# Kernel tuning notes

Hardware: AMD Instinct MI355X
Metric: run time of the kernel (lower is better)

## Reference

```python
import jax, jax.numpy as jnp
import numpy as np

B, T, I, H, P = 256, 2048, 2, 128, 129  # batch, max_len, input feats, hidden, num_pitches


def setup_inputs() -> dict:
    key = jax.random.key(0)
    ks = jax.random.split(key, 8)
    s = 1.0 / np.sqrt(H)  # torch LSTM/Linear init scale
    x = jax.random.normal(ks[0], (B, T, I), jnp.float32)
    lengths = jax.random.randint(ks[1], (B,), 1, T + 1, jnp.int32)
    W_ih = jax.random.uniform(ks[2], (4 * H, I), jnp.float32, -s, s)
    W_hh = jax.random.uniform(ks[3], (4 * H, H), jnp.float32, -s, s)
    note_W = jax.random.uniform(ks[4], (P, H), jnp.float32, -s, s)
    note_b = jax.random.uniform(ks[5], (P,), jnp.float32, -s, s)
    dur_W = jax.random.uniform(ks[6], (1, H), jnp.float32, -s, s)
    dur_b = jax.random.uniform(ks[7], (1,), jnp.float32, -s, s)
    return dict(x=x, lengths=lengths, W_ih=W_ih, W_hh=W_hh,
                note_W=note_W, note_b=note_b, dur_W=dur_W, dur_b=dur_b)


def _lstm(x, lengths, W_ih, W_hh):
    # Precompute input projections for all timesteps in one GEMM: [T,B,4H]
    pre = jnp.einsum('bti,gi->tbg', x, W_ih)
    h0 = jnp.zeros((x.shape[0], W_hh.shape[1]), x.dtype)
    c0 = h0
    ts = jnp.arange(x.shape[1])

    def step(carry, inp):
        h, c = carry
        px, t = inp
        gates = px + h @ W_hh.T  # [B,4H], torch gate order: i,f,g,o
        i_g, f_g, g_g, o_g = jnp.split(gates, 4, axis=-1)
        i_g = jax.nn.sigmoid(i_g)
        f_g = jax.nn.sigmoid(f_g)
        o_g = jax.nn.sigmoid(o_g)
        g_g = jnp.tanh(g_g)
        c_new = f_g * c + i_g * g_g
        h_new = o_g * jnp.tanh(c_new)
        m = (t < lengths)[:, None]  # packed semantics: freeze past length
        h2 = jnp.where(m, h_new, h)
        c2 = jnp.where(m, c_new, c)
        return (h2, c2), jnp.where(m, h_new, 0.0)

    (hT, cT), hs = jax.lax.scan(step, (h0, c0), (pre, ts))
    return jnp.transpose(hs, (1, 0, 2)), hT, cT  # [B,T,H], final states = states at last valid step


def reference(x, lengths, W_ih, W_hh, note_W, note_b, dur_W, dur_b):
    hs, hT, cT = _lstm(x, lengths, W_ih, W_hh)
    mask = (jnp.arange(x.shape[1])[None, :] < lengths[:, None])[..., None]
    note_logits = jnp.where(mask, hs @ note_W.T + note_b, 0.0)     # [B,T,129]
    duration_pred = jnp.where(mask, hs @ dur_W.T + dur_b, 0.0)     # [B,T,1]
    return note_logits, duration_pred, hT, cT
```

## Files before the change

### kernel.cpp

```cpp
#include <hip/hip_runtime.h>


typedef _Float16 f16;
typedef _Float16 f16x8 __attribute__((ext_vector_type(8)));
typedef float    f32x4 __attribute__((ext_vector_type(4)));

#define B_  256
#define T_  2048
#define H_  128
#define P_  129

static constexpr size_t NOTE_N   = (size_t)B_ * T_ * P_;
static constexpr size_t DUR_BASE = NOTE_N;
static constexpr size_t HT_BASE  = DUR_BASE + (size_t)B_ * T_;
static constexpr size_t CT_BASE  = HT_BASE + (size_t)B_ * H_;

#if defined(__has_builtin)
#if __has_builtin(__builtin_amdgcn_exp2f)
#define EXP2F(x) __builtin_amdgcn_exp2f(x)
#endif
#endif
#ifndef EXP2F
#define EXP2F(x) __expf((x) * 0.6931471805599453f)
#endif

__device__ __forceinline__ float fast_rcp(float x) { return __builtin_amdgcn_rcpf(x); }

__device__ __forceinline__ float sigmoid_f(float x) {
    float e = EXP2F(-1.44269504f * x);
    return fast_rcp(1.f + e);
}
__device__ __forceinline__ float tanh_f(float x) {
    float e = EXP2F(2.885390082f * x);
    return (e - 1.f) * fast_rcp(e + 1.f);
}

__device__ __forceinline__ f16* hs_row(float* out, int bt) {
    size_t byteoff = ((size_t)bt * (P_ * 4) + 15) & ~(size_t)15;
    return (f16*)((char*)out + byteoff);
}

__global__ __launch_bounds__(256) void prep_k(const float* __restrict__ note_W,
                                              const float* __restrict__ dur_W,
                                              f16* __restrict__ Wn) {
    int i = threadIdx.x + blockIdx.x * 256;
    if (i >= 144 * 128) return;
    int row = i >> 7, k = i & 127;
    float v = 0.f;
    if (row < 129)       v = note_W[row * 128 + k];
    else if (row == 129) v = dur_W[k];
    Wn[i] = (f16)v;
}

__global__ __launch_bounds__(256, 1) void lstm4_k(const float* __restrict__ x,
                                                  const int* __restrict__ lengths,
                                                  const float* __restrict__ W_ih,
                                                  const float* __restrict__ W_hh,
                                                  float* __restrict__ out) {
    __shared__ __align__(16) f16 h_sh[2][H_];
    __shared__ __align__(8) float2 xs[128];

    const int tid = threadIdx.x;
    const int b = blockIdx.x;
    const int w = tid >> 6;
    const int l = tid & 63;
    const int p = l & 15;
    const int q = l >> 4;
    const int sel = q >> 1;
    const int j = 16 * w + 64 * sel + p;
    const bool writer = ((q & 1) == 0);

    f16x8 Bf[8][4];
    float wxx[8], wxy[8];
#pragma unroll
    for (int s = 0; s < 8; s++) {
        const int c = 16 * (w + 4 * s) + p;
        const float* wr = W_hh + (size_t)c * H_ + 8 * q;
#pragma unroll
        for (int kt = 0; kt < 4; kt++) {
            float4 v1 = *(const float4*)(wr + 32 * kt);
            float4 v2 = *(const float4*)(wr + 32 * kt + 4);
            f16x8 f;
            f[0] = (f16)v1.x; f[1] = (f16)v1.y; f[2] = (f16)v1.z; f[3] = (f16)v1.w;
            f[4] = (f16)v2.x; f[5] = (f16)v2.y; f[6] = (f16)v2.z; f[7] = (f16)v2.w;
            Bf[s][kt] = f;
        }
        wxx[s] = W_ih[2 * c];
        wxy[s] = W_ih[2 * c + 1];
    }
    const int len = lengths[b];
    if (tid < 2 * H_) ((f16*)h_sh)[tid] = (f16)0.f;

    char* hp = (char*)out + (size_t)b * (T_ * 516ULL) + 2 * j;

    const f32x4 z4 = {0.f, 0.f, 0.f, 0.f};
    float c_reg = 0.f, h_reg = 0.f;

    for (int t = 0; t < len; t++) {
        if ((t & 127) == 0) {
            __syncthreads();
            if (tid < 128)
                xs[tid] = *(const float2*)(x + (size_t)b * T_ * 2 + (size_t)(t + tid) * 2);
            __syncthreads();
        }
        const int cur = t & 1;

        f16x8 Af[4];
#pragma unroll
        for (int kt = 0; kt < 4; kt++)
            Af[kt] = *(const f16x8*)(&h_sh[cur][32 * kt + 8 * q]);

        f32x4 acc[8];
#pragma unroll
        for (int s = 0; s < 8; s++)
            acc[s] = __builtin_amdgcn_mfma_f32_16x16x32_f16(Af[0], Bf[s][0], z4, 0, 0, 0);
#pragma unroll
        for (int kt = 1; kt < 4; kt++) {
#pragma unroll
            for (int s = 0; s < 8; s++)
                acc[s] = __builtin_amdgcn_mfma_f32_16x16x32_f16(
                    Af[kt], Bf[s][kt], acc[s], 0, 0, 0);
        }

        const float2 xv = xs[t & 127];
        float G[4];
#pragma unroll
        for (int tt = 0; tt < 4; tt++) {
            float ga = acc[2 * tt][0] +
                       __builtin_fmaf(wxy[2 * tt], xv.y, wxx[2 * tt] * xv.x);
            float gb = acc[2 * tt + 1][0] +
                       __builtin_fmaf(wxy[2 * tt + 1], xv.y, wxx[2 * tt + 1] * xv.x);
            G[tt] = sel ? gb : ga;
        }

        const float ig = sigmoid_f(G[0]);
        const float fg = sigmoid_f(G[1]);
        const float gg = tanh_f(G[2]);
        const float og = sigmoid_f(G[3]);
        c_reg = __builtin_fmaf(fg, c_reg, ig * gg);
        h_reg = og * tanh_f(fminf(fmaxf(c_reg, -15.f), 15.f));

        if (writer) {
            const f16 h16 = (f16)h_reg;
            h_sh[cur ^ 1][j] = h16;
            *(f16*)hp = h16;
        }
        hp += 512 + (((t & 3) == 0) ? 16 : 0);

        asm volatile("s_waitcnt lgkmcnt(0)" ::: "memory");
        __builtin_amdgcn_sched_barrier(0);
        __builtin_amdgcn_s_barrier();
        __builtin_amdgcn_sched_barrier(0);
    }

    if (writer) {
        out[HT_BASE + (size_t)b * H_ + j] = h_reg;
        out[CT_BASE + (size_t)b * H_ + j] = c_reg;
    }
}

__global__ __launch_bounds__(256) void proj_k(const int* __restrict__ lengths,
                                              const f16* __restrict__ Wn,
                                              const float* __restrict__ note_b,
                                              const float* __restrict__ dur_b,
                                              float* __restrict__ out) {
    __shared__ __align__(16) f16 wn_sh[144 * 136];

    const int tid = threadIdx.x;
    {
        unsigned int* dst = (unsigned int*)wn_sh;
        const unsigned int* src = (const unsigned int*)Wn;
        for (int w = tid; w < 144 * 64; w += 256) {
            int row = w >> 6, cw = w & 63;
            dst[row * 68 + cw] = src[w];
        }
    }
    __syncthreads();

    const int wv = tid >> 6;
    const int l = tid & 63;
    const int tile = blockIdx.x * 4 + wv;
    const int bt0 = tile * 16;
    const int b = bt0 >> 11;
    const int t0 = bt0 & 2047;
    const int len = lengths[b];
    const int r16 = l & 15, q = l >> 4;

    f32x4 acc[9];
#pragma unroll
    for (int nf = 0; nf < 9; nf++) acc[nf] = f32x4{0.f, 0.f, 0.f, 0.f};

    const bool live = (t0 < len);
    if (live) {
        f16x8 a[4];
        {
            const f16* ar = hs_row(out, bt0 + r16);
#pragma unroll
            for (int kk = 0; kk < 4; kk++)
                a[kk] = *(const f16x8*)(ar + kk * 32 + q * 8);
        }
#pragma unroll
        for (int nf = 0; nf < 9; nf++) {
            const f16* brow = wn_sh + (nf * 16 + r16) * 136 + q * 8;
#pragma unroll
            for (int kk = 0; kk < 4; kk++) {
                f16x8 bb = *(const f16x8*)(brow + kk * 32);
                acc[nf] = __builtin_amdgcn_mfma_f32_16x16x32_f16(a[kk], bb, acc[nf], 0, 0, 0);
            }
        }
    }

#pragma unroll
    for (int nf = 0; nf < 9; nf++) {
        int col = nf * 16 + r16;
        float bias = 0.f;
        if (col < 129)       bias = note_b[col];
        else if (col == 129) bias = dur_b[0];
#pragma unroll
        for (int r = 0; r < 4; r++) {
            int rowbt = bt0 + q * 4 + r;
            int t = t0 + q * 4 + r;
            float v = (t < len) ? (acc[nf][r] + bias) : 0.f;
            if (col < 129)
                out[(size_t)rowbt * P_ + col] = v;
            else if (col == 129)
                out[DUR_BASE + rowbt] = v;
        }
    }
}

extern "C" void kernel_launch(void* const* d_in, const int* in_sizes, int n_in,
                              void* d_out, int out_size, void* d_ws, size_t ws_size,
                              hipStream_t stream) {
    const float* x       = (const float*)d_in[0];
    const int*   lengths = (const int*)d_in[1];
    const float* W_ih    = (const float*)d_in[2];
    const float* W_hh    = (const float*)d_in[3];
    const float* note_W  = (const float*)d_in[4];
    const float* note_b  = (const float*)d_in[5];
    const float* dur_W   = (const float*)d_in[6];
    const float* dur_b   = (const float*)d_in[7];
    float* out = (float*)d_out;
    f16* Wn = (f16*)d_ws;

    prep_k<<<72, 256, 0, stream>>>(note_W, dur_W, Wn);
    lstm4_k<<<B_, 256, 0, stream>>>(x, lengths, W_ih, W_hh, out);
    proj_k<<<(B_ * T_) / 64, 256, 0, stream>>>(lengths, Wn, note_b, dur_b, out);
}
```

Measured before the change: 1.031 ms.

## Stage hidden states in a shared ring and flush 16-step blocks with vector stores

Replaces the per-step scalar 2-byte global stores of each hidden state with a 32-slot shared-memory ring. Every 16 steps, all threads flush one 16-step block to the hs scratch rows using 16-byte vector stores, and a tail flush handles the remainder. The ring also serves as the recurrent h double buffer. The x inputs are now prefetched one step ahead from global memory instead of being staged in shared memory every 128 steps, which removes those extra block barriers. The cost is a larger shared buffer and a periodic burst of stores inside the serial recurrence loop.

```diff
diff --git a/kernel.cpp b/kernel.cpp
--- a/kernel.cpp
+++ b/kernel.cpp
@@ -52,13 +52,12 @@
     Wn[i] = (f16)v;
 }
 
-__global__ __launch_bounds__(256, 1) void lstm4_k(const float* __restrict__ x,
+__global__ __launch_bounds__(256, 1) void lstm7_k(const float* __restrict__ x,
                                                   const int* __restrict__ lengths,
                                                   const float* __restrict__ W_ih,
                                                   const float* __restrict__ W_hh,
                                                   float* __restrict__ out) {
-    __shared__ __align__(16) f16 h_sh[2][H_];
-    __shared__ __align__(8) float2 xs[128];
+    __shared__ __align__(16) f16 hstage[32][136];
 
     const int tid = threadIdx.x;
     const int b = blockIdx.x;
@@ -89,26 +88,32 @@
         wxy[s] = W_ih[2 * c + 1];
     }
     const int len = lengths[b];
-    if (tid < 2 * H_) ((f16*)h_sh)[tid] = (f16)0.f;
-
-    char* hp = (char*)out + (size_t)b * (T_ * 516ULL) + 2 * j;
+
+    for (int i = tid; i < 32 * 136; i += 256) ((f16*)hstage)[i] = (f16)0.f;
+
+    const float2* xg = (const float2*)(x + (size_t)b * T_ * 2);
+    float2 xv = xg[0];
 
     const f32x4 z4 = {0.f, 0.f, 0.f, 0.f};
     float c_reg = 0.f, h_reg = 0.f;
+    __syncthreads();
 
     for (int t = 0; t < len; t++) {
-        if ((t & 127) == 0) {
-            __syncthreads();
-            if (tid < 128)
-                xs[tid] = *(const float2*)(x + (size_t)b * T_ * 2 + (size_t)(t + tid) * 2);
-            __syncthreads();
-        }
-        const int cur = t & 1;
-
+        const int tn = (t + 1 < len) ? (t + 1) : t;
+        float2 xnext = xg[tn];
+
+        if ((t & 15) == 0 && t) {
+            const int r = tid >> 4, ch = tid & 15;
+            const int step = t - 16 + r;
+            f16x8 v = *(const f16x8*)(&hstage[step & 31][ch * 8]);
+            *(f16x8*)(hs_row(out, b * T_ + step) + ch * 8) = v;
+        }
+
+        const int rprev = (t + 31) & 31;
         f16x8 Af[4];
 #pragma unroll
         for (int kt = 0; kt < 4; kt++)
-            Af[kt] = *(const f16x8*)(&h_sh[cur][32 * kt + 8 * q]);
+            Af[kt] = *(const f16x8*)(&hstage[rprev][32 * kt + 8 * q]);
 
         f32x4 acc[8];
 #pragma unroll
@@ -122,7 +127,6 @@
                     Af[kt], Bf[s][kt], acc[s], 0, 0, 0);
         }
 
-        const float2 xv = xs[t & 127];
         float G[4];
 #pragma unroll
         for (int tt = 0; tt < 4; tt++) {
@@ -140,17 +144,23 @@
         c_reg = __builtin_fmaf(fg, c_reg, ig * gg);
         h_reg = og * tanh_f(fminf(fmaxf(c_reg, -15.f), 15.f));
 
-        if (writer) {
-            const f16 h16 = (f16)h_reg;
-            h_sh[cur ^ 1][j] = h16;
-            *(f16*)hp = h16;
-        }
-        hp += 512 + (((t & 3) == 0) ? 16 : 0);
+        if (writer) hstage[t & 31][j] = (f16)h_reg;
+        xv = xnext;
 
         asm volatile("s_waitcnt lgkmcnt(0)" ::: "memory");
         __builtin_amdgcn_sched_barrier(0);
         __builtin_amdgcn_s_barrier();
         __builtin_amdgcn_sched_barrier(0);
+    }
+
+    {
+        const int tail = ((len - 1) >> 4) << 4;
+        const int r = tid >> 4, ch = tid & 15;
+        const int step = tail + r;
+        if (step < len) {
+            f16x8 v = *(const f16x8*)(&hstage[step & 31][ch * 8]);
+            *(f16x8*)(hs_row(out, b * T_ + step) + ch * 8) = v;
+        }
     }
 
     if (writer) {
@@ -244,6 +254,6 @@
     f16* Wn = (f16*)d_ws;
 
     prep_k<<<72, 256, 0, stream>>>(note_W, dur_W, Wn);
-    lstm4_k<<<B_, 256, 0, stream>>>(x, lengths, W_ih, W_hh, out);
+    lstm7_k<<<B_, 256, 0, stream>>>(x, lengths, W_ih, W_hh, out);
     proj_k<<<(B_ * T_) / 64, 256, 0, stream>>>(lengths, Wn, note_b, dur_b, out);
 }
```

Result: slower. 1.191 ms (+15.5%).
